# Kernel optimization log

Measured on AMD Instinct MI355X. Metric: run time of the kernel, lower is better.

The kernel has to match this reference:

```python
import jax, jax.numpy as jnp
import numpy as np

B, N, K, D, C, T_IN, T_OUT = 8, 500, 16, 32, 16, 12, 12


def setup_inputs() -> dict:
    key = jax.random.key(0)
    ks = jax.random.split(key, 10)
    s = 0.05
    return {
        "features": jax.random.normal(ks[0], (B, N, D), jnp.float32),
        "input_seq": jax.random.normal(ks[1], (B, N, T_IN), jnp.float32),
        "Wk": jax.random.normal(ks[2], (D, D), jnp.float32) * s,
        "bk": jnp.zeros((D,), jnp.float32),
        "Wq": jax.random.normal(ks[3], (D, D), jnp.float32) * s,
        "bq": jnp.zeros((D,), jnp.float32),
        "Wc": jax.random.normal(ks[4], (D, C), jnp.float32) * s,
        "bc": jnp.zeros((C,), jnp.float32),
        "Wcls": jax.random.normal(ks[5], (C, T_IN, T_OUT), jnp.float32) * s,
        "adj_topk_index": jax.random.randint(ks[6], (B, N, K), 0, N, jnp.int32),
    }


def reference(features, input_seq, Wk, bk, Wq, bq, Wc, bc, Wcls, adj_topk_index):
    # --- Nodes_Clustering_Learn: all-pairs key/query tanh attention -> class probs ---
    k = features @ Wk + bk                      # (B,N,D)
    q = features @ Wq + bq                      # (B,N,D)
    kq = jnp.tanh(k[:, :, None, :] + q[:, None, :, :])  # (B,N,N,D)
    probs = jax.nn.softmax(kq @ Wc + bc, axis=-1)        # (B,N,N,C)
    ids = jnp.argmax(probs, axis=-1)            # (B,N,N) cluster id of pair (i,j)

    # --- gather top-k neighbors per node (irregular access) ---
    ids_topk = jnp.take_along_axis(ids, adj_topk_index, axis=2)          # (B,N,K)
    x_topk = jax.vmap(lambda x, i: x[i])(input_seq, adj_topk_index)      # (B,N,K,T_IN)

    # --- Ordered_GCN: per-class masked mean over neighbors + per-class Linear+Tanh ---
    onehot = jax.nn.one_hot(ids_topk, C, dtype=x_topk.dtype)             # (B,N,K,C)
    summed = jnp.einsum('bnkc,bnkt->bnct', onehot, x_topk)               # (B,N,C,T_IN)
    count = onehot.sum(axis=2)                                           # (B,N,C)
    count = jnp.where(count == 0, jnp.ones_like(count), count)
    avg = summed / count[..., None]                                      # (B,N,C,T_IN)
    out = jnp.tanh(jnp.einsum('bnct,cto->bnco', avg, Wcls))              # (B,N,C,T_OUT)
    return out
```

## Files before the change

kernel.cpp:

```cpp
#include <hip/hip_runtime.h>
#include <math.h>

#define B 8
#define N 500
#define K 16
#define D 32
#define C 16
#define T_IN 12
#define T_OUT 12
#define NNODE (B * N)

__global__ __launch_bounds__(256) void compute_kq(
    const float* __restrict__ features,
    const float* __restrict__ Wk,
    const float* __restrict__ bk,
    const float* __restrict__ Wq,
    const float* __restrict__ bq,
    float* __restrict__ kq)
{
    const int tid = threadIdx.x;
    __shared__ float s_W[2][D * D];
    __shared__ float s_b[2][D];
    __shared__ float s_f[4][D];

    #pragma unroll
    for (int i = 0; i < 4; ++i) s_W[0][tid + i * 256] = Wk[tid + i * 256];
    #pragma unroll
    for (int i = 0; i < 4; ++i) s_W[1][tid + i * 256] = Wq[tid + i * 256];
    if (tid < D) { s_b[0][tid] = bk[tid]; s_b[1][tid] = bq[tid]; }
    if (tid < 4 * D)
        s_f[tid >> 5][tid & 31] =
            features[(size_t)(blockIdx.x * 4 + (tid >> 5)) * D + (tid & 31)];
    __syncthreads();

    const int local = tid >> 6;
    const int lane  = tid & 63;
    const int d     = lane & 31;
    const int m     = lane >> 5;
    float acc = s_b[m][d];
    #pragma unroll
    for (int e = 0; e < D; ++e) acc += s_f[local][e] * s_W[m][e * D + d];
    kq[(size_t)(blockIdx.x * 4 + local) * 64 + lane] = acc;
}

__global__ __launch_bounds__(256) void embed_gcn_fused(
    const float* __restrict__ input_seq,
    const float* __restrict__ Wc,
    const float* __restrict__ bc,
    const float* __restrict__ Wcls,
    const int*   __restrict__ adj,
    const float* __restrict__ kq,
    float* __restrict__ out)
{
    const int tid  = threadIdx.x;
    const int w    = tid >> 6;
    const int l    = tid & 63;
    const int s    = l & 3;
    const int g    = l >> 2;
    const int node = blockIdx.x * 4 + w;
    const int b    = node / N;

    __shared__ __align__(16) float s_Wc[D * C];
    __shared__ __align__(16) float s_Wcls[C * T_IN * T_OUT];
    __shared__ float s_bc[C];
    __shared__ __align__(16) float s_k[4][D];
    __shared__ __align__(16) float s_t[4][K][36];
    __shared__ __align__(16) float s_x[4][K][T_IN];
    __shared__ float s_avg[4][C][T_IN];
    __shared__ int   s_id[4][K];
    __shared__ int   s_adj[4][K];

    s_Wc[tid]       = Wc[tid];
    s_Wc[tid + 256] = Wc[tid + 256];
    #pragma unroll
    for (int i = 0; i < 9; ++i) s_Wcls[tid + i * 256] = Wcls[tid + i * 256];
    if (tid < C) s_bc[tid] = bc[tid];
    if (l < K) s_adj[w][l] = adj[(size_t)node * K + l];
    if (l < D) s_k[w][l] = kq[(size_t)node * 64 + l];
    __syncthreads();

    const int j  = s_adj[w][g];
    const int jn = b * N + j;
    const float4 q0 = *(const float4*)&kq[(size_t)jn * 64 + 32 + s * 8];
    const float4 q1 = *(const float4*)&kq[(size_t)jn * 64 + 32 + s * 8 + 4];
    float4 x4;
    if (s < 3) x4 = *(const float4*)&input_seq[(size_t)jn * T_IN + s * 4];
    const float4 k0 = *(const float4*)&s_k[w][s * 8];
    const float4 k1 = *(const float4*)&s_k[w][s * 8 + 4];

    float4 t0, t1;
    t0.x = tanhf(k0.x + q0.x);  t0.y = tanhf(k0.y + q0.y);
    t0.z = tanhf(k0.z + q0.z);  t0.w = tanhf(k0.w + q0.w);
    t1.x = tanhf(k1.x + q1.x);  t1.y = tanhf(k1.y + q1.y);
    t1.z = tanhf(k1.z + q1.z);  t1.w = tanhf(k1.w + q1.w);
    *(float4*)&s_t[w][g][s * 8]     = t0;
    *(float4*)&s_t[w][g][s * 8 + 4] = t1;
    if (s < 3) *(float4*)&s_x[w][g][s * 4] = x4;
    __syncthreads();

    float a0 = s_bc[s * 4 + 0];
    float a1 = s_bc[s * 4 + 1];
    float a2 = s_bc[s * 4 + 2];
    float a3 = s_bc[s * 4 + 3];
    #pragma unroll
    for (int ch = 0; ch < 8; ++ch) {
        const float4 t4 = *(const float4*)&s_t[w][g][ch * 4];
        const float tv[4] = { t4.x, t4.y, t4.z, t4.w };
        #pragma unroll
        for (int dd = 0; dd < 4; ++dd) {
            const int d = ch * 4 + dd;
            const float4 w4 = *(const float4*)&s_Wc[d * C + s * 4];
            a0 += tv[dd] * w4.x;
            a1 += tv[dd] * w4.y;
            a2 += tv[dd] * w4.z;
            a3 += tv[dd] * w4.w;
        }
    }

    float m = fmaxf(fmaxf(a0, a1), fmaxf(a2, a3));
    m = fmaxf(m, __shfl_xor(m, 1, 4));
    m = fmaxf(m, __shfl_xor(m, 2, 4));
    const float e0 = expf(a0 - m), e1 = expf(a1 - m);
    const float e2 = expf(a2 - m), e3 = expf(a3 - m);
    float sum = e0 + e1 + e2 + e3;
    sum += __shfl_xor(sum, 1, 4);
    sum += __shfl_xor(sum, 2, 4);
    const float p0 = e0 / sum, p1 = e1 / sum, p2 = e2 / sum, p3 = e3 / sum;

    float bp = p0; int bi = s * 4;
    if (p1 > bp) { bp = p1; bi = s * 4 + 1; }
    if (p2 > bp) { bp = p2; bi = s * 4 + 2; }
    if (p3 > bp) { bp = p3; bi = s * 4 + 3; }
    #pragma unroll
    for (int off = 1; off <= 2; off <<= 1) {
        const float op = __shfl_xor(bp, off, 4);
        const int   oi = __shfl_xor(bi, off, 4);
        if (op > bp || (op == bp && oi < bi)) { bp = op; bi = oi; }
    }
    if (s == 0) s_id[w][g] = bi;
    __syncthreads();

    int ids[K];
    #pragma unroll
    for (int kk = 0; kk < K; ++kk) ids[kk] = s_id[w][kk];
    #pragma unroll
    for (int it = 0; it < 3; ++it) {
        const int id2 = l + it * 64;
        const int cc  = id2 / T_IN;
        const int t   = id2 - cc * T_IN;
        float sm = 0.f; int cnt = 0;
        #pragma unroll
        for (int kk = 0; kk < K; ++kk) {
            const bool hit = (ids[kk] == cc);
            const float xv = s_x[w][kk][t];
            if (hit) { sm += xv; ++cnt; }
        }
        s_avg[w][cc][t] = sm / (float)(cnt ? cnt : 1);
    }
    __syncthreads();

    #pragma unroll
    for (int it = 0; it < 3; ++it) {
        const int id2 = l + it * 64;
        const int cc  = id2 / T_OUT;
        const int o   = id2 - cc * T_OUT;
        float acc = 0.f;
        #pragma unroll
        for (int t = 0; t < T_IN; ++t)
            acc += s_avg[w][cc][t] * s_Wcls[cc * (T_IN * T_OUT) + t * T_OUT + o];
        out[(size_t)node * (C * T_OUT) + id2] = tanhf(acc);
    }
}

extern "C" void kernel_launch(void* const* d_in, const int* in_sizes, int n_in,
                              void* d_out, int out_size, void* d_ws, size_t ws_size,
                              hipStream_t stream) {
    const float* features  = (const float*)d_in[0];
    const float* input_seq = (const float*)d_in[1];
    const float* Wk        = (const float*)d_in[2];
    const float* bk        = (const float*)d_in[3];
    const float* Wq        = (const float*)d_in[4];
    const float* bq        = (const float*)d_in[5];
    const float* Wc        = (const float*)d_in[6];
    const float* bc        = (const float*)d_in[7];
    const float* Wcls      = (const float*)d_in[8];
    const int*   adj       = (const int*)d_in[9];
    float*       out       = (float*)d_out;
    float*       kq        = (float*)d_ws;

    compute_kq<<<NNODE / 4, 256, 0, stream>>>(features, Wk, bk, Wq, bq, kq);
    embed_gcn_fused<<<NNODE / 4, 256, 0, stream>>>(input_seq, Wc, bc, Wcls, adj, kq, out);
}
```

Measured before the change: 19.17 us.

## Fuse key/query projection into the GCN kernel and drop inter-stage barriers

Merges the separate key/query projection kernel into the main kernel, so there is one launch and no key/query workspace written to and read back from global memory. Each wave computes its own node's key projection and, per neighbor, recomputes the query projection from gathered feature rows. That recomputation is redundant across nodes that share neighbors. Weight staging switches to float4 loads, and the block-wide __syncthreads between stages are removed, relying on each node's data being produced and consumed within a single wave; this leans on wave-level LDS ordering without explicit barriers.

```diff
diff --git a/kernel.cpp b/kernel.cpp
--- a/kernel.cpp
+++ b/kernel.cpp
@@ -10,46 +10,17 @@
 #define T_OUT 12
 #define NNODE (B * N)
 
-__global__ __launch_bounds__(256) void compute_kq(
+__global__ __launch_bounds__(256) void embed_gcn_one(
     const float* __restrict__ features,
+    const float* __restrict__ input_seq,
     const float* __restrict__ Wk,
     const float* __restrict__ bk,
     const float* __restrict__ Wq,
     const float* __restrict__ bq,
-    float* __restrict__ kq)
-{
-    const int tid = threadIdx.x;
-    __shared__ float s_W[2][D * D];
-    __shared__ float s_b[2][D];
-    __shared__ float s_f[4][D];
-
-    #pragma unroll
-    for (int i = 0; i < 4; ++i) s_W[0][tid + i * 256] = Wk[tid + i * 256];
-    #pragma unroll
-    for (int i = 0; i < 4; ++i) s_W[1][tid + i * 256] = Wq[tid + i * 256];
-    if (tid < D) { s_b[0][tid] = bk[tid]; s_b[1][tid] = bq[tid]; }
-    if (tid < 4 * D)
-        s_f[tid >> 5][tid & 31] =
-            features[(size_t)(blockIdx.x * 4 + (tid >> 5)) * D + (tid & 31)];
-    __syncthreads();
-
-    const int local = tid >> 6;
-    const int lane  = tid & 63;
-    const int d     = lane & 31;
-    const int m     = lane >> 5;
-    float acc = s_b[m][d];
-    #pragma unroll
-    for (int e = 0; e < D; ++e) acc += s_f[local][e] * s_W[m][e * D + d];
-    kq[(size_t)(blockIdx.x * 4 + local) * 64 + lane] = acc;
-}
-
-__global__ __launch_bounds__(256) void embed_gcn_fused(
-    const float* __restrict__ input_seq,
     const float* __restrict__ Wc,
     const float* __restrict__ bc,
     const float* __restrict__ Wcls,
     const int*   __restrict__ adj,
-    const float* __restrict__ kq,
     float* __restrict__ out)
 {
     const int tid  = threadIdx.x;
@@ -60,104 +31,142 @@
     const int node = blockIdx.x * 4 + w;
     const int b    = node / N;
 
+    __shared__ __align__(16) float s_Wk[D * D];
+    __shared__ __align__(16) float s_Wq[D * D];
     __shared__ __align__(16) float s_Wc[D * C];
     __shared__ __align__(16) float s_Wcls[C * T_IN * T_OUT];
-    __shared__ float s_bc[C];
+    __shared__ float s_bk[D], s_bq[D], s_bc[C];
+    __shared__ __align__(16) float s_fo[4][D];
+    __shared__ __align__(16) float s_ft[4][K][36];
+    __shared__ __align__(16) float s_x[4][K][T_IN];
     __shared__ __align__(16) float s_k[4][D];
-    __shared__ __align__(16) float s_t[4][K][36];
-    __shared__ __align__(16) float s_x[4][K][T_IN];
     __shared__ float s_avg[4][C][T_IN];
     __shared__ int   s_id[4][K];
-    __shared__ int   s_adj[4][K];
-
-    s_Wc[tid]       = Wc[tid];
-    s_Wc[tid + 256] = Wc[tid + 256];
-    #pragma unroll
-    for (int i = 0; i < 9; ++i) s_Wcls[tid + i * 256] = Wcls[tid + i * 256];
+    __shared__ int   s_adj[4 * K];
+
+    if (tid < 64) s_adj[tid] = adj[(size_t)blockIdx.x * 64 + tid];
+    *(float4*)&s_Wk[tid * 4] = *(const float4*)&Wk[tid * 4];
+    *(float4*)&s_Wq[tid * 4] = *(const float4*)&Wq[tid * 4];
+    if (tid < 128) *(float4*)&s_Wc[tid * 4] = *(const float4*)&Wc[tid * 4];
+    *(float4*)&s_Wcls[tid * 4]         = *(const float4*)&Wcls[tid * 4];
+    *(float4*)&s_Wcls[1024 + tid * 4]  = *(const float4*)&Wcls[1024 + tid * 4];
+    if (tid < 64) *(float4*)&s_Wcls[2048 + tid * 4] = *(const float4*)&Wcls[2048 + tid * 4];
+    if (tid < D) { s_bk[tid] = bk[tid]; s_bq[tid] = bq[tid]; }
     if (tid < C) s_bc[tid] = bc[tid];
-    if (l < K) s_adj[w][l] = adj[(size_t)node * K + l];
-    if (l < D) s_k[w][l] = kq[(size_t)node * 64 + l];
+    if (tid < 32) *(float4*)&s_fo[0][tid * 4] =
+        *(const float4*)&features[(size_t)blockIdx.x * 128 + tid * 4];
     __syncthreads();
 
-    const int j  = s_adj[w][g];
+    const int j  = s_adj[w * 16 + g];
     const int jn = b * N + j;
-    const float4 q0 = *(const float4*)&kq[(size_t)jn * 64 + 32 + s * 8];
-    const float4 q1 = *(const float4*)&kq[(size_t)jn * 64 + 32 + s * 8 + 4];
+    const float* __restrict__ fj = &features[(size_t)jn * D];
+    const float4 f0 = *(const float4*)&fj[s * 8];
+    const float4 f1 = *(const float4*)&fj[s * 8 + 4];
     float4 x4;
     if (s < 3) x4 = *(const float4*)&input_seq[(size_t)jn * T_IN + s * 4];
-    const float4 k0 = *(const float4*)&s_k[w][s * 8];
-    const float4 k1 = *(const float4*)&s_k[w][s * 8 + 4];
-
-    float4 t0, t1;
-    t0.x = tanhf(k0.x + q0.x);  t0.y = tanhf(k0.y + q0.y);
-    t0.z = tanhf(k0.z + q0.z);  t0.w = tanhf(k0.w + q0.w);
-    t1.x = tanhf(k1.x + q1.x);  t1.y = tanhf(k1.y + q1.y);
-    t1.z = tanhf(k1.z + q1.z);  t1.w = tanhf(k1.w + q1.w);
-    *(float4*)&s_t[w][g][s * 8]     = t0;
-    *(float4*)&s_t[w][g][s * 8 + 4] = t1;
+
+    if (l < D) {
+        float acc = s_bk[l];
+        #pragma unroll
+        for (int e = 0; e < D; ++e) acc += s_fo[w][e] * s_Wk[e * D + l];
+        s_k[w][l] = acc;
+    }
+
+    *(float4*)&s_ft[w][g][s * 8]     = f0;
+    *(float4*)&s_ft[w][g][s * 8 + 4] = f1;
     if (s < 3) *(float4*)&s_x[w][g][s * 4] = x4;
-    __syncthreads();
-
-    float a0 = s_bc[s * 4 + 0];
-    float a1 = s_bc[s * 4 + 1];
-    float a2 = s_bc[s * 4 + 2];
-    float a3 = s_bc[s * 4 + 3];
-    #pragma unroll
-    for (int ch = 0; ch < 8; ++ch) {
-        const float4 t4 = *(const float4*)&s_t[w][g][ch * 4];
-        const float tv[4] = { t4.x, t4.y, t4.z, t4.w };
-        #pragma unroll
-        for (int dd = 0; dd < 4; ++dd) {
-            const int d = ch * 4 + dd;
-            const float4 w4 = *(const float4*)&s_Wc[d * C + s * 4];
-            a0 += tv[dd] * w4.x;
-            a1 += tv[dd] * w4.y;
-            a2 += tv[dd] * w4.z;
-            a3 += tv[dd] * w4.w;
-        }
-    }
-
-    float m = fmaxf(fmaxf(a0, a1), fmaxf(a2, a3));
-    m = fmaxf(m, __shfl_xor(m, 1, 4));
-    m = fmaxf(m, __shfl_xor(m, 2, 4));
-    const float e0 = expf(a0 - m), e1 = expf(a1 - m);
-    const float e2 = expf(a2 - m), e3 = expf(a3 - m);
-    float sum = e0 + e1 + e2 + e3;
-    sum += __shfl_xor(sum, 1, 4);
-    sum += __shfl_xor(sum, 2, 4);
-    const float p0 = e0 / sum, p1 = e1 / sum, p2 = e2 / sum, p3 = e3 / sum;
-
-    float bp = p0; int bi = s * 4;
-    if (p1 > bp) { bp = p1; bi = s * 4 + 1; }
-    if (p2 > bp) { bp = p2; bi = s * 4 + 2; }
-    if (p3 > bp) { bp = p3; bi = s * 4 + 3; }
-    #pragma unroll
-    for (int off = 1; off <= 2; off <<= 1) {
-        const float op = __shfl_xor(bp, off, 4);
-        const int   oi = __shfl_xor(bi, off, 4);
-        if (op > bp || (op == bp && oi < bi)) { bp = op; bi = oi; }
-    }
-    if (s == 0) s_id[w][g] = bi;
-    __syncthreads();
-
-    int ids[K];
-    #pragma unroll
-    for (int kk = 0; kk < K; ++kk) ids[kk] = s_id[w][kk];
-    #pragma unroll
-    for (int it = 0; it < 3; ++it) {
-        const int id2 = l + it * 64;
-        const int cc  = id2 / T_IN;
-        const int t   = id2 - cc * T_IN;
-        float sm = 0.f; int cnt = 0;
-        #pragma unroll
-        for (int kk = 0; kk < K; ++kk) {
-            const bool hit = (ids[kk] == cc);
-            const float xv = s_x[w][kk][t];
-            if (hit) { sm += xv; ++cnt; }
-        }
-        s_avg[w][cc][t] = sm / (float)(cnt ? cnt : 1);
-    }
-    __syncthreads();
+
+    {
+        float q[8];
+        #pragma unroll
+        for (int dd = 0; dd < 8; ++dd) q[dd] = s_bq[s * 8 + dd];
+        #pragma unroll
+        for (int e4 = 0; e4 < D; e4 += 4) {
+            const float4 f = *(const float4*)&s_ft[w][g][e4];
+            const float fv[4] = { f.x, f.y, f.z, f.w };
+            #pragma unroll
+            for (int ee = 0; ee < 4; ++ee) {
+                const int e = e4 + ee;
+                const float4 wa = *(const float4*)&s_Wq[e * D + s * 8];
+                const float4 wb = *(const float4*)&s_Wq[e * D + s * 8 + 4];
+                q[0] += fv[ee] * wa.x;  q[1] += fv[ee] * wa.y;
+                q[2] += fv[ee] * wa.z;  q[3] += fv[ee] * wa.w;
+                q[4] += fv[ee] * wb.x;  q[5] += fv[ee] * wb.y;
+                q[6] += fv[ee] * wb.z;  q[7] += fv[ee] * wb.w;
+            }
+        }
+        float t[8];
+        #pragma unroll
+        for (int dd = 0; dd < 8; ++dd)
+            t[dd] = tanhf(s_k[w][s * 8 + dd] + q[dd]);
+        float4 t0 = { t[0], t[1], t[2], t[3] };
+        float4 t1 = { t[4], t[5], t[6], t[7] };
+        *(float4*)&s_ft[w][g][s * 8]     = t0;
+        *(float4*)&s_ft[w][g][s * 8 + 4] = t1;
+    }
+
+    {
+        float a0 = s_bc[s * 4 + 0];
+        float a1 = s_bc[s * 4 + 1];
+        float a2 = s_bc[s * 4 + 2];
+        float a3 = s_bc[s * 4 + 3];
+        #pragma unroll
+        for (int ch = 0; ch < 8; ++ch) {
+            const float4 t4 = *(const float4*)&s_ft[w][g][ch * 4];
+            const float tv[4] = { t4.x, t4.y, t4.z, t4.w };
+            #pragma unroll
+            for (int dd = 0; dd < 4; ++dd) {
+                const int d = ch * 4 + dd;
+                const float4 w4 = *(const float4*)&s_Wc[d * C + s * 4];
+                a0 += tv[dd] * w4.x;
+                a1 += tv[dd] * w4.y;
+                a2 += tv[dd] * w4.z;
+                a3 += tv[dd] * w4.w;
+            }
+        }
+
+        float m = fmaxf(fmaxf(a0, a1), fmaxf(a2, a3));
+        m = fmaxf(m, __shfl_xor(m, 1, 4));
+        m = fmaxf(m, __shfl_xor(m, 2, 4));
+        const float e0 = expf(a0 - m), e1 = expf(a1 - m);
+        const float e2 = expf(a2 - m), e3 = expf(a3 - m);
+        float sum = e0 + e1 + e2 + e3;
+        sum += __shfl_xor(sum, 1, 4);
+        sum += __shfl_xor(sum, 2, 4);
+        const float p0 = e0 / sum, p1 = e1 / sum, p2 = e2 / sum, p3 = e3 / sum;
+
+        float bp = p0; int bi = s * 4;
+        if (p1 > bp) { bp = p1; bi = s * 4 + 1; }
+        if (p2 > bp) { bp = p2; bi = s * 4 + 2; }
+        if (p3 > bp) { bp = p3; bi = s * 4 + 3; }
+        #pragma unroll
+        for (int off = 1; off <= 2; off <<= 1) {
+            const float op = __shfl_xor(bp, off, 4);
+            const int   oi = __shfl_xor(bi, off, 4);
+            if (op > bp || (op == bp && oi < bi)) { bp = op; bi = oi; }
+        }
+        if (s == 0) s_id[w][g] = bi;
+    }
+
+    {
+        int ids[K];
+        #pragma unroll
+        for (int kk = 0; kk < K; ++kk) ids[kk] = s_id[w][kk];
+        #pragma unroll
+        for (int it = 0; it < 3; ++it) {
+            const int id2 = l + it * 64;
+            const int cc  = id2 / T_IN;
+            const int t   = id2 - cc * T_IN;
+            float sm = 0.f; int cnt = 0;
+            #pragma unroll
+            for (int kk = 0; kk < K; ++kk) {
+                const bool hit = (ids[kk] == cc);
+                const float xv = s_x[w][kk][t];
+                if (hit) { sm += xv; ++cnt; }
+            }
+            s_avg[w][cc][t] = sm / (float)(cnt ? cnt : 1);
+        }
+    }
 
     #pragma unroll
     for (int it = 0; it < 3; ++it) {
@@ -186,8 +195,7 @@
     const float* Wcls      = (const float*)d_in[8];
     const int*   adj       = (const int*)d_in[9];
     float*       out       = (float*)d_out;
-    float*       kq        = (float*)d_ws;
-
-    compute_kq<<<NNODE / 4, 256, 0, stream>>>(features, Wk, bk, Wq, bq, kq);
-    embed_gcn_fused<<<NNODE / 4, 256, 0, stream>>>(input_seq, Wc, bc, Wcls, adj, kq, out);
+
+    embed_gcn_one<<<NNODE / 4, 256, 0, stream>>>(
+        features, input_seq, Wk, bk, Wq, bq, Wc, bc, Wcls, adj, out);
 }
```

Measured after the change: 35.70 us. +86.2%, slower.

## Replace LDS staging and block barriers with DPP quad broadcasts and reductions

Applied to the files above, without the earlier changes.

The fused GCN kernel no longer stages Wc, Wcls, adjacency and the tanh vectors in shared memory behind block-wide barriers. It broadcasts tanh values across each 4-lane quad with DPP quad_perm, reads the weights straight from global/L2, and keeps only small per-wave LDS buffers that each 64-lane wavefront writes and reads itself with no __syncthreads. The Wcls matmul is split across quad lanes over the time dimension and summed with DPP swaps. compute_kq now handles 16 nodes per block using float4 loads and stores. The aim is to cut barrier stalls and the shared-memory weight loads each block repeats. The cost is more register pressure and the reliance on wavefront-synchronous LDS use.

```diff
diff --git a/kernel.cpp b/kernel.cpp
--- a/kernel.cpp
+++ b/kernel.cpp
@@ -9,6 +9,12 @@
 #define T_IN 12
 #define T_OUT 12
 #define NNODE (B * N)
+
+template <int CTRL>
+__device__ __forceinline__ float qperm(float v) {
+    return __int_as_float(__builtin_amdgcn_update_dpp(
+        0, __float_as_int(v), CTRL, 0xF, 0xF, true));
+}
 
 __global__ __launch_bounds__(256) void compute_kq(
     const float* __restrict__ features,
@@ -19,31 +25,43 @@
     float* __restrict__ kq)
 {
     const int tid = threadIdx.x;
-    __shared__ float s_W[2][D * D];
-    __shared__ float s_b[2][D];
-    __shared__ float s_f[4][D];
-
+    __shared__ __align__(16) float s_W[2][D * D];
+    __shared__ __align__(16) float s_f[16][36];
+
+    {
+        const float4 wk4 = *(const float4*)&Wk[tid * 4];
+        const float4 wq4 = *(const float4*)&Wq[tid * 4];
+        *(float4*)&s_W[0][tid * 4] = wk4;
+        *(float4*)&s_W[1][tid * 4] = wq4;
+    }
+    if (tid < 128) {
+        const int n  = tid >> 3;
+        const int e4 = tid & 7;
+        *(float4*)&s_f[n][e4 * 4] =
+            *(const float4*)&features[(size_t)blockIdx.x * 512 + tid * 4];
+    }
+    __syncthreads();
+
+    const int n  = tid >> 4;
+    const int m  = (tid >> 3) & 1;
+    const int d4 = tid & 7;
+    const float* __restrict__ bias = m ? bq : bk;
+    float4 acc = *(const float4*)&bias[d4 * 4];
     #pragma unroll
-    for (int i = 0; i < 4; ++i) s_W[0][tid + i * 256] = Wk[tid + i * 256];
-    #pragma unroll
-    for (int i = 0; i < 4; ++i) s_W[1][tid + i * 256] = Wq[tid + i * 256];
-    if (tid < D) { s_b[0][tid] = bk[tid]; s_b[1][tid] = bq[tid]; }
-    if (tid < 4 * D)
-        s_f[tid >> 5][tid & 31] =
-            features[(size_t)(blockIdx.x * 4 + (tid >> 5)) * D + (tid & 31)];
-    __syncthreads();
-
-    const int local = tid >> 6;
-    const int lane  = tid & 63;
-    const int d     = lane & 31;
-    const int m     = lane >> 5;
-    float acc = s_b[m][d];
-    #pragma unroll
-    for (int e = 0; e < D; ++e) acc += s_f[local][e] * s_W[m][e * D + d];
-    kq[(size_t)(blockIdx.x * 4 + local) * 64 + lane] = acc;
-}
-
-__global__ __launch_bounds__(256) void embed_gcn_fused(
+    for (int e4 = 0; e4 < 8; ++e4) {
+        const float4 f = *(const float4*)&s_f[n][e4 * 4];
+        const float fv[4] = { f.x, f.y, f.z, f.w };
+        #pragma unroll
+        for (int ee = 0; ee < 4; ++ee) {
+            const float4 w4 = *(const float4*)&s_W[m][(e4 * 4 + ee) * D + d4 * 4];
+            acc.x += fv[ee] * w4.x;  acc.y += fv[ee] * w4.y;
+            acc.z += fv[ee] * w4.z;  acc.w += fv[ee] * w4.w;
+        }
+    }
+    *(float4*)&kq[(size_t)(blockIdx.x * 16 + n) * 64 + m * 32 + d4 * 4] = acc;
+}
+
+__global__ __launch_bounds__(256) void embed_gcn(
     const float* __restrict__ input_seq,
     const float* __restrict__ Wc,
     const float* __restrict__ bc,
@@ -60,115 +78,153 @@
     const int node = blockIdx.x * 4 + w;
     const int b    = node / N;
 
-    __shared__ __align__(16) float s_Wc[D * C];
-    __shared__ __align__(16) float s_Wcls[C * T_IN * T_OUT];
-    __shared__ float s_bc[C];
-    __shared__ __align__(16) float s_k[4][D];
-    __shared__ __align__(16) float s_t[4][K][36];
-    __shared__ __align__(16) float s_x[4][K][T_IN];
-    __shared__ float s_avg[4][C][T_IN];
-    __shared__ int   s_id[4][K];
-    __shared__ int   s_adj[4][K];
-
-    s_Wc[tid]       = Wc[tid];
-    s_Wc[tid + 256] = Wc[tid + 256];
-    #pragma unroll
-    for (int i = 0; i < 9; ++i) s_Wcls[tid + i * 256] = Wcls[tid + i * 256];
-    if (tid < C) s_bc[tid] = bc[tid];
-    if (l < K) s_adj[w][l] = adj[(size_t)node * K + l];
-    if (l < D) s_k[w][l] = kq[(size_t)node * 64 + l];
-    __syncthreads();
-
-    const int j  = s_adj[w][g];
+    __shared__ __align__(16) float s_xT[4][T_IN][16];
+    __shared__ __align__(16) int   s_id[4][16];
+
+    const int j  = adj[(size_t)node * K + g];
     const int jn = b * N + j;
     const float4 q0 = *(const float4*)&kq[(size_t)jn * 64 + 32 + s * 8];
-    const float4 q1 = *(const float4*)&kq[(size_t)jn * 64 + 32 + s * 8 + 4];
-    float4 x4;
-    if (s < 3) x4 = *(const float4*)&input_seq[(size_t)jn * T_IN + s * 4];
-    const float4 k0 = *(const float4*)&s_k[w][s * 8];
-    const float4 k1 = *(const float4*)&s_k[w][s * 8 + 4];
-
-    float4 t0, t1;
-    t0.x = tanhf(k0.x + q0.x);  t0.y = tanhf(k0.y + q0.y);
-    t0.z = tanhf(k0.z + q0.z);  t0.w = tanhf(k0.w + q0.w);
-    t1.x = tanhf(k1.x + q1.x);  t1.y = tanhf(k1.y + q1.y);
-    t1.z = tanhf(k1.z + q1.z);  t1.w = tanhf(k1.w + q1.w);
-    *(float4*)&s_t[w][g][s * 8]     = t0;
-    *(float4*)&s_t[w][g][s * 8 + 4] = t1;
-    if (s < 3) *(float4*)&s_x[w][g][s * 4] = x4;
-    __syncthreads();
-
-    float a0 = s_bc[s * 4 + 0];
-    float a1 = s_bc[s * 4 + 1];
-    float a2 = s_bc[s * 4 + 2];
-    float a3 = s_bc[s * 4 + 3];
+    const float4 q1 = *(const float4*)&kq[(size_t)jn * 64 + 36 + s * 8];
+    const float4 k0 = *(const float4*)&kq[(size_t)node * 64 + s * 8];
+    const float4 k1 = *(const float4*)&kq[(size_t)node * 64 + s * 8 + 4];
+    if (s < 3) {
+        const float4 x4 = *(const float4*)&input_seq[(size_t)jn * T_IN + s * 4];
+        s_xT[w][s * 4 + 0][g] = x4.x;
+        s_xT[w][s * 4 + 1][g] = x4.y;
+        s_xT[w][s * 4 + 2][g] = x4.z;
+        s_xT[w][s * 4 + 3][g] = x4.w;
+    }
+    const float t0 = tanhf(k0.x + q0.x), t1 = tanhf(k0.y + q0.y);
+    const float t2 = tanhf(k0.z + q0.z), t3 = tanhf(k0.w + q0.w);
+    const float t4 = tanhf(k1.x + q1.x), t5 = tanhf(k1.y + q1.y);
+    const float t6 = tanhf(k1.z + q1.z), t7 = tanhf(k1.w + q1.w);
+
+    float tc0[8], tc1[8], tc2[8], tc3[8];
+#define BC(dst, CTRL) \
+    dst[0] = qperm<CTRL>(t0); dst[1] = qperm<CTRL>(t1); \
+    dst[2] = qperm<CTRL>(t2); dst[3] = qperm<CTRL>(t3); \
+    dst[4] = qperm<CTRL>(t4); dst[5] = qperm<CTRL>(t5); \
+    dst[6] = qperm<CTRL>(t6); dst[7] = qperm<CTRL>(t7);
+    BC(tc0, 0x00)  BC(tc1, 0x55)  BC(tc2, 0xAA)  BC(tc3, 0xFF)
+#undef BC
+
+    {
+        const float4 bc4 = *(const float4*)&bc[s * 4];
+        float a0 = bc4.x, a1 = bc4.y, a2 = bc4.z, a3 = bc4.w;
+        const float* __restrict__ wcp = Wc + s * 4;
+        #pragma unroll
+        for (int i = 0; i < 8; ++i) {
+            const float4 w4 = *(const float4*)&wcp[(i) * C];
+            a0 += tc0[i] * w4.x; a1 += tc0[i] * w4.y; a2 += tc0[i] * w4.z; a3 += tc0[i] * w4.w;
+        }
+        #pragma unroll
+        for (int i = 0; i < 8; ++i) {
+            const float4 w4 = *(const float4*)&wcp[(8 + i) * C];
+            a0 += tc1[i] * w4.x; a1 += tc1[i] * w4.y; a2 += tc1[i] * w4.z; a3 += tc1[i] * w4.w;
+        }
+        #pragma unroll
+        for (int i = 0; i < 8; ++i) {
+            const float4 w4 = *(const float4*)&wcp[(16 + i) * C];
+            a0 += tc2[i] * w4.x; a1 += tc2[i] * w4.y; a2 += tc2[i] * w4.z; a3 += tc2[i] * w4.w;
+        }
+        #pragma unroll
+        for (int i = 0; i < 8; ++i) {
+            const float4 w4 = *(const float4*)&wcp[(24 + i) * C];
+            a0 += tc3[i] * w4.x; a1 += tc3[i] * w4.y; a2 += tc3[i] * w4.z; a3 += tc3[i] * w4.w;
+        }
+
+        float m = fmaxf(fmaxf(a0, a1), fmaxf(a2, a3));
+        m = fmaxf(m, __shfl_xor(m, 1, 4));
+        m = fmaxf(m, __shfl_xor(m, 2, 4));
+        const float e0 = expf(a0 - m), e1 = expf(a1 - m);
+        const float e2 = expf(a2 - m), e3 = expf(a3 - m);
+        float sum = e0 + e1 + e2 + e3;
+        sum += __shfl_xor(sum, 1, 4);
+        sum += __shfl_xor(sum, 2, 4);
+        const float p0 = e0 / sum, p1 = e1 / sum, p2 = e2 / sum, p3 = e3 / sum;
+
+        float bp = p0; int bi = s * 4;
+        if (p1 > bp) { bp = p1; bi = s * 4 + 1; }
+        if (p2 > bp) { bp = p2; bi = s * 4 + 2; }
+        if (p3 > bp) { bp = p3; bi = s * 4 + 3; }
+        #pragma unroll
+        for (int off = 1; off <= 2; off <<= 1) {
+            const float op = __shfl_xor(bp, off, 4);
+            const int   oi = __shfl_xor(bi, off, 4);
+            if (op > bp || (op == bp && oi < bi)) { bp = op; bi = oi; }
+        }
+        if (s == 0) s_id[w][g] = bi;
+    }
+
+    const int cc = l >> 2;
+    const int tq = l & 3;
+    const int tbase = tq * 3;
+
+    const int4 i0 = *(const int4*)&s_id[w][0];
+    const int4 i1 = *(const int4*)&s_id[w][4];
+    const int4 i2 = *(const int4*)&s_id[w][8];
+    const int4 i3 = *(const int4*)&s_id[w][12];
+    float msk[16]; int cnt = 0;
+    {
+        const int idv[16] = { i0.x, i0.y, i0.z, i0.w,  i1.x, i1.y, i1.z, i1.w,
+                              i2.x, i2.y, i2.z, i2.w,  i3.x, i3.y, i3.z, i3.w };
+        #pragma unroll
+        for (int kk = 0; kk < 16; ++kk) {
+            const bool h = (idv[kk] == cc);
+            msk[kk] = h ? 1.f : 0.f;
+            cnt += h;
+        }
+    }
+    const float fcnt = (cnt == 0) ? 1.f : (float)cnt;
+
+    float av0, av1, av2;
+#define CELL(avx, T) { \
+    const float4 xa = *(const float4*)&s_xT[w][T][0]; \
+    const float4 xb = *(const float4*)&s_xT[w][T][4]; \
+    const float4 xc = *(const float4*)&s_xT[w][T][8]; \
+    const float4 xd = *(const float4*)&s_xT[w][T][12]; \
+    float sm = 0.f; \
+    sm += msk[0]*xa.x;  sm += msk[1]*xa.y;  sm += msk[2]*xa.z;  sm += msk[3]*xa.w; \
+    sm += msk[4]*xb.x;  sm += msk[5]*xb.y;  sm += msk[6]*xb.z;  sm += msk[7]*xb.w; \
+    sm += msk[8]*xc.x;  sm += msk[9]*xc.y;  sm += msk[10]*xc.z; sm += msk[11]*xc.w; \
+    sm += msk[12]*xd.x; sm += msk[13]*xd.y; sm += msk[14]*xd.z; sm += msk[15]*xd.w; \
+    avx = sm / fcnt; }
+    CELL(av0, tbase)  CELL(av1, tbase + 1)  CELL(av2, tbase + 2)
+#undef CELL
+
+    const float* __restrict__ wcl = Wcls + ((size_t)cc * T_IN + tbase) * T_OUT;
+    float p[12];
+    {
+        const float4 wA0 = *(const float4*)&wcl[0];
+        const float4 wA1 = *(const float4*)&wcl[4];
+        const float4 wA2 = *(const float4*)&wcl[8];
+        p[0] = av0 * wA0.x;  p[1] = av0 * wA0.y;  p[2]  = av0 * wA0.z;  p[3]  = av0 * wA0.w;
+        p[4] = av0 * wA1.x;  p[5] = av0 * wA1.y;  p[6]  = av0 * wA1.z;  p[7]  = av0 * wA1.w;
+        p[8] = av0 * wA2.x;  p[9] = av0 * wA2.y;  p[10] = av0 * wA2.z;  p[11] = av0 * wA2.w;
+        const float4 wB0 = *(const float4*)&wcl[12];
+        const float4 wB1 = *(const float4*)&wcl[16];
+        const float4 wB2 = *(const float4*)&wcl[20];
+        p[0] += av1 * wB0.x;  p[1] += av1 * wB0.y;  p[2]  += av1 * wB0.z;  p[3]  += av1 * wB0.w;
+        p[4] += av1 * wB1.x;  p[5] += av1 * wB1.y;  p[6]  += av1 * wB1.z;  p[7]  += av1 * wB1.w;
+        p[8] += av1 * wB2.x;  p[9] += av1 * wB2.y;  p[10] += av1 * wB2.z;  p[11] += av1 * wB2.w;
+        const float4 wC0 = *(const float4*)&wcl[24];
+        const float4 wC1 = *(const float4*)&wcl[28];
+        const float4 wC2 = *(const float4*)&wcl[32];
+        p[0] += av2 * wC0.x;  p[1] += av2 * wC0.y;  p[2]  += av2 * wC0.z;  p[3]  += av2 * wC0.w;
+        p[4] += av2 * wC1.x;  p[5] += av2 * wC1.y;  p[6]  += av2 * wC1.z;  p[7]  += av2 * wC1.w;
+        p[8] += av2 * wC2.x;  p[9] += av2 * wC2.y;  p[10] += av2 * wC2.z;  p[11] += av2 * wC2.w;
+    }
     #pragma unroll
-    for (int ch = 0; ch < 8; ++ch) {
-        const float4 t4 = *(const float4*)&s_t[w][g][ch * 4];
-        const float tv[4] = { t4.x, t4.y, t4.z, t4.w };
-        #pragma unroll
-        for (int dd = 0; dd < 4; ++dd) {
-            const int d = ch * 4 + dd;
-            const float4 w4 = *(const float4*)&s_Wc[d * C + s * 4];
-            a0 += tv[dd] * w4.x;
-            a1 += tv[dd] * w4.y;
-            a2 += tv[dd] * w4.z;
-            a3 += tv[dd] * w4.w;
-        }
-    }
-
-    float m = fmaxf(fmaxf(a0, a1), fmaxf(a2, a3));
-    m = fmaxf(m, __shfl_xor(m, 1, 4));
-    m = fmaxf(m, __shfl_xor(m, 2, 4));
-    const float e0 = expf(a0 - m), e1 = expf(a1 - m);
-    const float e2 = expf(a2 - m), e3 = expf(a3 - m);
-    float sum = e0 + e1 + e2 + e3;
-    sum += __shfl_xor(sum, 1, 4);
-    sum += __shfl_xor(sum, 2, 4);
-    const float p0 = e0 / sum, p1 = e1 / sum, p2 = e2 / sum, p3 = e3 / sum;
-
-    float bp = p0; int bi = s * 4;
-    if (p1 > bp) { bp = p1; bi = s * 4 + 1; }
-    if (p2 > bp) { bp = p2; bi = s * 4 + 2; }
-    if (p3 > bp) { bp = p3; bi = s * 4 + 3; }
+    for (int o = 0; o < 12; ++o) {
+        p[o] += qperm<0xB1>(p[o]);
+        p[o] += qperm<0x4E>(p[o]);
+    }
     #pragma unroll
-    for (int off = 1; off <= 2; off <<= 1) {
-        const float op = __shfl_xor(bp, off, 4);
-        const int   oi = __shfl_xor(bi, off, 4);
-        if (op > bp || (op == bp && oi < bi)) { bp = op; bi = oi; }
-    }
-    if (s == 0) s_id[w][g] = bi;
-    __syncthreads();
-
-    int ids[K];
-    #pragma unroll
-    for (int kk = 0; kk < K; ++kk) ids[kk] = s_id[w][kk];
-    #pragma unroll
-    for (int it = 0; it < 3; ++it) {
-        const int id2 = l + it * 64;
-        const int cc  = id2 / T_IN;
-        const int t   = id2 - cc * T_IN;
-        float sm = 0.f; int cnt = 0;
-        #pragma unroll
-        for (int kk = 0; kk < K; ++kk) {
-            const bool hit = (ids[kk] == cc);
-            const float xv = s_x[w][kk][t];
-            if (hit) { sm += xv; ++cnt; }
-        }
-        s_avg[w][cc][t] = sm / (float)(cnt ? cnt : 1);
-    }
-    __syncthreads();
-
-    #pragma unroll
-    for (int it = 0; it < 3; ++it) {
-        const int id2 = l + it * 64;
-        const int cc  = id2 / T_OUT;
-        const int o   = id2 - cc * T_OUT;
-        float acc = 0.f;
-        #pragma unroll
-        for (int t = 0; t < T_IN; ++t)
-            acc += s_avg[w][cc][t] * s_Wcls[cc * (T_IN * T_OUT) + t * T_OUT + o];
-        out[(size_t)node * (C * T_OUT) + id2] = tanhf(acc);
+    for (int i = 0; i < 3; ++i) {
+        const float va = (tq & 1) ? p[3 + i] : p[i];
+        const float vb = (tq & 1) ? p[9 + i] : p[6 + i];
+        const float v  = (tq & 2) ? vb : va;
+        out[(size_t)node * (C * T_OUT) + cc * T_OUT + tbase + i] = tanhf(v);
     }
 }
 
@@ -188,6 +244,6 @@
     float*       out       = (float*)d_out;
     float*       kq        = (float*)d_ws;
 
-    compute_kq<<<NNODE / 4, 256, 0, stream>>>(features, Wk, bk, Wq, bq, kq);
-    embed_gcn_fused<<<NNODE / 4, 256, 0, stream>>>(input_seq, Wc, bc, Wcls, adj, kq, out);
-}
+    compute_kq<<<NNODE / 16, 256, 0, stream>>>(features, Wk, bk, Wq, bq, kq);
+    embed_gcn<<<NNODE / 4, 256, 0, stream>>>(input_seq, Wc, bc, Wcls, adj, kq, out);
+}
```

New measurement: 19.36 us. About the same (+1.0%).
